# Performance work log

Hardware: AMD Instinct MI355X
Metric: run time of the kernel (lower is better)

## Reference

```python
import math
import jax, jax.numpy as jnp
import numpy as np

H = 8          # n_heads (params['h'])
TOPK_K = 2     # params['k']
TAU = 25       # moving-average window (params['tau'])


def ma_decomp(x, tau):
    """MADecompositionLayer: edge-pad by tau, centered moving average of width tau."""
    B, L, D = x.shape
    front = jnp.repeat(x[:, :1], tau, axis=1)
    back = jnp.repeat(x[:, -1:], tau, axis=1)
    padded = jnp.concatenate([front, x, back], axis=1)          # (B, L+2tau, D)
    cs = jnp.cumsum(padded, axis=1)
    cs = jnp.concatenate([jnp.zeros_like(cs[:, :1]), cs], axis=1)
    off = tau - (tau - 1) // 2  # start offset of the SAME-padded pool window
    trend = (cs[:, off + tau: off + tau + L] - cs[:, off: off + L]) / tau
    return x - trend, trend     # (seasonality, trend)


def corr_attention(x, Wq, bq, Wk, bk, Wv, bv, Wo, bo):
    """CorrLayer (inference path: per-sample top-k delay aggregation)."""
    B, L, D = x.shape
    dk = D // H
    # projections -> (B, h, d, L)
    q = (x @ Wq + bq).reshape(B, L, H, dk).transpose(0, 2, 3, 1)
    k = (x @ Wk + bk).reshape(B, L, H, dk).transpose(0, 2, 3, 1)
    v = (x @ Wv + bv).reshape(B, L, H, dk).transpose(0, 2, 3, 1)
    # FFT cross-correlation as written in the source:
    # corr = irfft(real = qr*kr, imag = -(qi*ki))
    qf = jnp.fft.rfft(q, axis=-1)
    kf = jnp.fft.rfft(k, axis=-1)
    spec = (qf.real * kf.real) - 1j * (qf.imag * kf.imag)
    corr = jnp.fft.irfft(spec, n=L, axis=-1)                    # (B, h, d, L)
    # top-k delay selection per sample
    top_k = min(int(TOPK_K * math.log(L)), L)
    mean_value = corr.mean(axis=(1, 2))                          # (B, L)
    weights, delay = jax.lax.top_k(mean_value, top_k)            # (B, topk)
    w = jax.nn.softmax(weights, axis=-1)                         # (B, topk)
    # circular-shift gather: values[..., (delay + arange(L)) % L]
    idx = (delay[:, :, None] + jnp.arange(L)[None, None, :]) % L  # (B, topk, L)
    rolled = jnp.take_along_axis(v[:, None], idx[:, :, None, None, :], axis=-1)  # (B, topk, h, d, L)
    agg = jnp.einsum('bt,bthdl->bhdl', w, rolled)                # (B, h, d, L)
    out = agg.transpose(0, 3, 1, 2).reshape(B, L, H * dk)        # (B, L, D)
    return out @ Wo + bo


def setup_inputs() -> dict:
    key = jax.random.key(0)
    ks = jax.random.split(key, 8)
    B, L, D, DFF = 8, 2048, 512, 2048
    s = 0.02
    return {
        'x':  jax.random.normal(ks[0], (B, L, D), jnp.float32),
        'Wq': jax.random.normal(ks[1], (D, D), jnp.float32) * s,
        'bq': jnp.zeros((D,), jnp.float32),
        'Wk': jax.random.normal(ks[2], (D, D), jnp.float32) * s,
        'bk': jnp.zeros((D,), jnp.float32),
        'Wv': jax.random.normal(ks[3], (D, D), jnp.float32) * s,
        'bv': jnp.zeros((D,), jnp.float32),
        'Wo': jax.random.normal(ks[4], (D, D), jnp.float32) * s,
        'bo': jnp.zeros((D,), jnp.float32),
        'W1': jax.random.normal(ks[5], (D, DFF), jnp.float32) * s,
        'W2': jax.random.normal(ks[6], (DFF, D), jnp.float32) * s,
    }


def reference(x, Wq, bq, Wk, bk, Wv, bv, Wo, bo, W1, W2):
    # Autoformer encoder layer: attn + residual, decomp, FFN, decomp
    attn_out = corr_attention(x, Wq, bq, Wk, bk, Wv, bv, Wo, bo)
    xr = x + attn_out                       # dropout_rate = 0.0
    s1, _ = ma_decomp(xr, TAU)
    y = jax.nn.relu(s1 @ W1) @ W2           # FFN (bias-free, as in Autoformer conv1d)
    s2, _ = ma_decomp(s1 + y, TAU)
    return s2
```

## Files before the change

### kernel.cpp

```cpp
#include <hip/hip_runtime.h>
#include <math.h>

namespace {
constexpr int kB = 8;
constexpr int kL = 2048;
constexpr int kD = 512;
constexpr int kTopk = 15;
constexpr int kLMask = 2047;
}

typedef unsigned short u16;
using f32x4 = __attribute__((ext_vector_type(4))) float;
using bf16x8 = __attribute__((ext_vector_type(8))) __bf16;

__device__ __forceinline__ u16 f2b(float f) {
  unsigned u = __float_as_uint(f);
  unsigned r = (u + 0x7fffu + ((u >> 16) & 1u)) >> 16;
  return (u16)r;
}
__device__ __forceinline__ float b2f(u16 u) {
  return __uint_as_float(((unsigned)u) << 16);
}

typedef __attribute__((address_space(3))) unsigned int lds_u32;
typedef __attribute__((address_space(1))) const unsigned int glb_u32;
__device__ __forceinline__ void gl2lds16(const void* g, void* l) {
  __builtin_amdgcn_global_load_lds((glb_u32*)g, (lds_u32*)l, 16, 0, 0);
}

template <int SPLIT, int RELU, int OUTF, int OUTB, int RES>
__global__ __launch_bounds__(256)
void mfma_gemm(const u16* __restrict__ A, const u16* __restrict__ Bt,
               const float* __restrict__ bias, const float* __restrict__ ResF,
               const u16* __restrict__ ResB, float* __restrict__ outF,
               u16* __restrict__ outB, int N, int K, int lda, int ldb, int nbn) {
  __shared__ u16 As[128 * 64];
  __shared__ u16 Bs[128 * 64];
  int lin = blockIdx.x;
  int split = 0;
  if (SPLIT) { split = lin >> 9; lin &= 511; }
  const int xcd = lin & 7;
  const int s = lin >> 3;
  const int q = s / nbn;
  const int bm = xcd * 16 + q;
  const int bn = s - q * nbn;
  const int tid = threadIdx.x;
  const int wave = tid >> 6;
  const int lane = tid & 63;
  const int ln = lane & 15;
  const int quad = lane >> 4;
  const int wm = (wave >> 1) * 64;
  const int wn = (wave & 1) * 64;
  const int srow = tid >> 3;
  const int scol = (tid & 7) * 8;

  const size_t koff = (size_t)split * K;
  const u16* Ab = A + koff + (size_t)(bm * 128) * lda + scol;
  const u16* Bb = Bt + koff + (size_t)(bn * 128) * ldb + scol;
  char* ldsA = (char*)As + wave * 1024;
  char* ldsB = (char*)Bs + wave * 1024;

  f32x4 acc[4][4];
#pragma unroll
  for (int i = 0; i < 4; ++i)
#pragma unroll
    for (int j = 0; j < 4; ++j) acc[i][j] = (f32x4){0.f, 0.f, 0.f, 0.f};

  for (int k0 = 0; k0 < K; k0 += 64) {
#pragma unroll
    for (int c = 0; c < 4; ++c) {
      gl2lds16(Ab + (size_t)(srow + 32 * c) * lda + k0, ldsA + c * 4096);
      gl2lds16(Bb + (size_t)(srow + 32 * c) * ldb + k0, ldsB + c * 4096);
    }
    __syncthreads();
#pragma unroll
    for (int kk = 0; kk < 2; ++kk) {
      bf16x8 af[4], bfr[4];
#pragma unroll
      for (int i = 0; i < 4; ++i)
        af[i] = *(const bf16x8*)(As + (wm + i * 16 + ln) * 64 + kk * 32 + quad * 8);
#pragma unroll
      for (int j = 0; j < 4; ++j)
        bfr[j] = *(const bf16x8*)(Bs + (wn + j * 16 + ln) * 64 + kk * 32 + quad * 8);
#pragma unroll
      for (int i = 0; i < 4; ++i)
#pragma unroll
        for (int j = 0; j < 4; ++j)
          acc[i][j] = __builtin_amdgcn_mfma_f32_16x16x32_bf16(bfr[j], af[i], acc[i][j], 0, 0, 0);
    }
    __syncthreads();
  }

  const size_t cbase = (size_t)split * ((size_t)16384 * N);
  const bool res2 = (RES == 2) && (!SPLIT || split == 0);
#pragma unroll
  for (int i = 0; i < 4; ++i) {
    const int row = bm * 128 + wm + i * 16 + ln;
#pragma unroll
    for (int j = 0; j < 4; ++j) {
      const int col = bn * 128 + wn + j * 16 + quad * 4;
      f32x4 v = acc[i][j];
      if (bias) {
        float4 bv = *(const float4*)(bias + col);
        v[0] += bv.x; v[1] += bv.y; v[2] += bv.z; v[3] += bv.w;
      }
      if (RES == 1) {
        float4 rv = *(const float4*)(ResF + (size_t)row * N + col);
        v[0] += rv.x; v[1] += rv.y; v[2] += rv.z; v[3] += rv.w;
      }
      if (RES == 2) {
        if (res2) {
          ushort4 rv = *(const ushort4*)(ResB + (size_t)row * N + col);
          v[0] += b2f(rv.x); v[1] += b2f(rv.y); v[2] += b2f(rv.z); v[3] += b2f(rv.w);
        }
      }
      if (RELU) {
#pragma unroll
        for (int r = 0; r < 4; ++r) v[r] = fmaxf(v[r], 0.f);
      }
      if (OUTF) {
        float4 o = {v[0], v[1], v[2], v[3]};
        *(float4*)(outF + cbase + (size_t)row * N + col) = o;
      }
      if (OUTB) {
        ushort4 o = {f2b(v[0]), f2b(v[1]), f2b(v[2]), f2b(v[3])};
        *(ushort4*)(outB + cbase + (size_t)row * N + col) = o;
      }
    }
  }
}

#define RDA(BUF, I, KK) \
  (*(const bf16x8*)&sm[BUF][0][arow + (I) * 1024 + ((KK) ? cx1 : cx0)])
#define RDB(BUF, J, KK) \
  (*(const bf16x8*)&sm[BUF][1][brow + (J) * 1024 + ((KK) ? cx1 : cx0)])
#define STAGE_A(BUF, Q, T) \
  gl2lds16(Ab + (size_t)(Q) * 64 * lda + (size_t)(T) * 64, \
           &sm[BUF][0][((Q) * 64 + wave * 8) * 64])
#define STAGE_B(BUF, Q, T) \
  gl2lds16(Bb + (size_t)(Q) * 64 * ldb + (size_t)(T) * 64, \
           &sm[BUF][1][((Q) * 64 + wave * 8) * 64])
#define MFMA1(i, j, kk, areg) \
  acc[i][j] = __builtin_amdgcn_mfma_f32_16x16x32_bf16(bf[j][kk], areg, acc[i][j], 0, 0, 0)
#define PHASE_MFMA(I0, A0k0, A0k1, A1k0, A1k1)                                 \
  MFMA1(I0, 0, 0, A0k0); MFMA1(I0, 1, 0, A0k0);                                \
  MFMA1(I0, 2, 0, A0k0); MFMA1(I0, 3, 0, A0k0);                                \
  MFMA1((I0) + 1, 0, 0, A1k0); MFMA1((I0) + 1, 1, 0, A1k0);                    \
  MFMA1((I0) + 1, 2, 0, A1k0); MFMA1((I0) + 1, 3, 0, A1k0);                    \
  MFMA1(I0, 0, 1, A0k1); MFMA1(I0, 1, 1, A0k1);                                \
  MFMA1(I0, 2, 1, A0k1); MFMA1(I0, 3, 1, A0k1);                                \
  MFMA1((I0) + 1, 0, 1, A1k1); MFMA1((I0) + 1, 1, 1, A1k1);                    \
  MFMA1((I0) + 1, 2, 1, A1k1); MFMA1((I0) + 1, 3, 1, A1k1)

#define GTILE(CUR, T)                                                          \
  {                                                                            \
    constexpr int NXT = (CUR) ^ 1;                                             \
    const bool hn = (T) + 1 < NT;                                              \
    const int tn = (T) + 1;                                                    \
    bf16x8 bf[4][2];                                                           \
    {                                                             \
      bf16x8 a00 = RDA(CUR, 0, 0), a01 = RDA(CUR, 0, 1);                       \
      bf16x8 a10 = RDA(CUR, 1, 0), a11 = RDA(CUR, 1, 1);                       \
      bf[0][0] = RDB(CUR, 0, 0); bf[0][1] = RDB(CUR, 0, 1);                    \
      bf[1][0] = RDB(CUR, 1, 0); bf[1][1] = RDB(CUR, 1, 1);                    \
      bf[2][0] = RDB(CUR, 2, 0); bf[2][1] = RDB(CUR, 2, 1);                    \
      bf[3][0] = RDB(CUR, 3, 0); bf[3][1] = RDB(CUR, 3, 1);                    \
      if (hn) { STAGE_B(NXT, 0, tn); STAGE_B(NXT, 1, tn); }                    \
      asm volatile("s_barrier" ::: "memory");                                  \
      __builtin_amdgcn_s_setprio(1);                                           \
      PHASE_MFMA(0, a00, a01, a10, a11);                                       \
      __builtin_amdgcn_s_setprio(0);                                           \
      asm volatile("s_barrier" ::: "memory");                                  \
    }                                                                          \
    {                                                             \
      bf16x8 a00 = RDA(CUR, 2, 0), a01 = RDA(CUR, 2, 1);                       \
      bf16x8 a10 = RDA(CUR, 3, 0), a11 = RDA(CUR, 3, 1);                       \
      if (hn) { STAGE_B(NXT, 2, tn); STAGE_B(NXT, 3, tn); }                    \
      asm volatile("s_barrier" ::: "memory");                                  \
      __builtin_amdgcn_s_setprio(1);                                           \
      PHASE_MFMA(2, a00, a01, a10, a11);                                       \
      __builtin_amdgcn_s_setprio(0);                                           \
      if (hn) { asm volatile("s_waitcnt vmcnt(4)" ::: "memory"); }             \
      else    { asm volatile("s_waitcnt vmcnt(0)" ::: "memory"); }             \
      asm volatile("s_barrier" ::: "memory");                                  \
    }                                                                          \
    {                                                             \
      bf16x8 a00 = RDA(CUR, 4, 0), a01 = RDA(CUR, 4, 1);                       \
      bf16x8 a10 = RDA(CUR, 5, 0), a11 = RDA(CUR, 5, 1);                       \
      if (hn) { STAGE_A(NXT, 0, tn); STAGE_A(NXT, 2, tn); }                    \
      asm volatile("s_barrier" ::: "memory");                                  \
      __builtin_amdgcn_s_setprio(1);                                           \
      PHASE_MFMA(4, a00, a01, a10, a11);                                       \
      __builtin_amdgcn_s_setprio(0);                                           \
      asm volatile("s_barrier" ::: "memory");                                  \
    }                                                                          \
    {                                                             \
      bf16x8 a00 = RDA(CUR, 6, 0), a01 = RDA(CUR, 6, 1);                       \
      bf16x8 a10 = RDA(CUR, 7, 0), a11 = RDA(CUR, 7, 1);                       \
      if (hn) { STAGE_A(NXT, 1, tn); STAGE_A(NXT, 3, tn); }                    \
      asm volatile("s_barrier" ::: "memory");                                  \
      __builtin_amdgcn_s_setprio(1);                                           \
      PHASE_MFMA(6, a00, a01, a10, a11);                                       \
      __builtin_amdgcn_s_setprio(0);                                           \
      if (hn) { asm volatile("s_waitcnt vmcnt(2)" ::: "memory"); }             \
      asm volatile("s_barrier" ::: "memory");                                  \
    }                                                                          \
  }

template <int SPLITK, int RELU, int HAS_BIAS, int OUTF, int RES>
__global__ __launch_bounds__(512, 2)
void gemm256(const u16* __restrict__ A, const u16* __restrict__ Bt,
             const float* __restrict__ bias, const u16* __restrict__ ResB,
             u16* __restrict__ outB, float* __restrict__ outF,
             int N, int K, int lda, int ldb, int nbn) {
  __shared__ u16 sm[2][2][256 * 64];
  const int lin = blockIdx.x;
  int bm, bn, split = 0;
  if (SPLITK) {
    const int xcd = lin & 7;
    const int s = lin >> 3;
    bm = xcd * 8 + (s & 7);
    bn = (s >> 3) & 1;
    split = s >> 4;
  } else {
    const int chunk = (int)gridDim.x >> 3;
    const int gid = (lin & 7) * chunk + (lin >> 3);
    bm = gid / nbn;
    bn = gid - bm * nbn;
  }

  const int tid = threadIdx.x;
  const int wave = tid >> 6;
  const int lane = tid & 63;
  const int ln = lane & 15;
  const int quad = lane >> 4;
  const int wm = (wave >> 2) * 128;
  const int wn = (wave & 3) * 64;

  const int srow = tid >> 3;
  const int schunk = (tid & 7) ^ (srow & 7);

  const size_t koff = (size_t)split * K;
  const u16* Ab = A + koff + (size_t)(bm * 256 + srow) * lda + schunk * 8;
  const u16* Bb = Bt + koff + (size_t)(bn * 256 + srow) * ldb + schunk * 8;

  const int cx0 = ((quad) ^ (ln & 7)) * 8;
  const int cx1 = ((4 | quad) ^ (ln & 7)) * 8;
  const int arow = (wm + ln) * 64;
  const int brow = (wn + ln) * 64;

  const int NT = K >> 6;

  f32x4 acc[8][4];
#pragma unroll
  for (int i = 0; i < 8; ++i)
#pragma unroll
    for (int j = 0; j < 4; ++j) acc[i][j] = (f32x4){0.f, 0.f, 0.f, 0.f};

  STAGE_B(0, 0, 0); STAGE_B(0, 1, 0); STAGE_B(0, 2, 0); STAGE_B(0, 3, 0);
  STAGE_A(0, 0, 0); STAGE_A(0, 2, 0); STAGE_A(0, 1, 0); STAGE_A(0, 3, 0);
  asm volatile("s_waitcnt vmcnt(2)" ::: "memory");
  asm volatile("s_barrier" ::: "memory");

  for (int t = 0; t < NT; t += 2) {
    GTILE(0, t);
    GTILE(1, t + 1);
  }

  const int col0 = bn * 256 + wn + quad * 4;
  const size_t cbase = (size_t)split * ((size_t)16384 * N);
#pragma unroll
  for (int i = 0; i < 8; ++i) {
    const size_t row = (size_t)(bm * 256 + wm + i * 16 + ln);
#pragma unroll
    for (int j = 0; j < 4; ++j) {
      const int col = col0 + j * 16;
      f32x4 v = acc[i][j];
      if (HAS_BIAS) {
        float4 bv = *(const float4*)(bias + col);
        v[0] += bv.x; v[1] += bv.y; v[2] += bv.z; v[3] += bv.w;
      }
      if (RES == 2) {
        if (split == 0) {
          ushort4 rv = *(const ushort4*)(ResB + row * N + col);
          v[0] += b2f(rv.x); v[1] += b2f(rv.y); v[2] += b2f(rv.z); v[3] += b2f(rv.w);
        }
      }
      if (RELU) {
        v[0] = fmaxf(v[0], 0.f); v[1] = fmaxf(v[1], 0.f);
        v[2] = fmaxf(v[2], 0.f); v[3] = fmaxf(v[3], 0.f);
      }
      if (OUTF) {
        float4 o = {v[0], v[1], v[2], v[3]};
        *(float4*)(outF + cbase + row * N + col) = o;
      } else {
        ushort4 o = {f2b(v[0]), f2b(v[1]), f2b(v[2]), f2b(v[3])};
        *(ushort4*)(outB + row * N + col) = o;
      }
    }
  }
}

#undef RDA
#undef RDB
#undef STAGE_A
#undef STAGE_B
#undef MFMA1
#undef PHASE_MFMA
#undef GTILE

__global__ __launch_bounds__(256)
void fft_corr(const u16* __restrict__ qkv, float* __restrict__ pA,
              float* __restrict__ pB) {
  __shared__ u16 stq[4 * 2048];
  __shared__ u16 stk[4 * 2048];
  __shared__ float re[2048];
  __shared__ float im[2048];
  const int blk = blockIdx.x;
  const int b = blk & 7;
  const int g = blk >> 3;
  const int t = threadIdx.x;
  const float PI = 3.14159265358979323846f;

  const u16* qb = qkv + (size_t)b * kL * 1536 + g * 4;
#pragma unroll
  for (int p = 0; p < 8; ++p) {
    const int row = p * 256 + t;
    *(ushort4*)&stq[row * 4] = *(const ushort4*)(qb + (size_t)row * 1536);
    *(ushort4*)&stk[row * 4] = *(const ushort4*)(qb + (size_t)row * 1536 + 512);
  }

  const int r = t & 31;
  float cA[4], sA[4], cB[2], sB[2], cC, sC;
  float cD[4], sD[4], cE[2], sE[2], cF, sF;
#pragma unroll
  for (int j = 0; j < 4; ++j)
    __sincosf(PI * (float)(t + 256 * j) * (1.f / 1024.f), &sA[j], &cA[j]);
#pragma unroll
  for (int j = 0; j < 2; ++j)
    __sincosf(PI * (float)(t + 256 * j) * (1.f / 512.f), &sB[j], &cB[j]);
  __sincosf(PI * (float)t * (1.f / 256.f), &sC, &cC);
#pragma unroll
  for (int j = 0; j < 4; ++j)
    __sincosf(PI * (float)(r + 32 * j) * (1.f / 128.f), &sD[j], &cD[j]);
#pragma unroll
  for (int j = 0; j < 2; ++j)
    __sincosf(PI * (float)(r + 32 * j) * (1.f / 64.f), &sE[j], &cE[j]);
  __sincosf(PI * (float)r * (1.f / 32.f), &sF, &cF);
  float sgn[5], cS[5], sS[5];
#pragma unroll
  for (int k = 0; k < 5; ++k) {
    const int m = 16 >> k;
    const bool hi = (t & m) != 0;
    float sv, cv;
    __sincosf(PI * (float)(t & (m - 1)) / (float)m, &sv, &cv);
    sgn[k] = hi ? -1.f : 1.f;
    cS[k] = hi ? cv : 1.f;
    sS[k] = hi ? sv : 0.f;
  }

  float accA[8], accB[8];
#pragma unroll
  for (int i = 0; i < 8; ++i) { accA[i] = 0.f; accB[i] = 0.f; }

  const int base2 = (t >> 5) * 256 + r;

#define BFLY(X, Y, CV, SV)                                              \
  { const float dr_ = er[X] - er[Y], di_ = ei[X] - ei[Y];               \
    er[X] += er[Y]; ei[X] += ei[Y];                                     \
    er[Y] = dr_ * (CV) + di_ * (SV); ei[Y] = di_ * (CV) - dr_ * (SV); }

#pragma unroll
  for (int c = 0; c < 4; ++c) {
    __syncthreads();
    float er[8], ei[8];
#pragma unroll
    for (int j = 0; j < 8; ++j) {
      er[j] = b2f(stq[(t + 256 * j) * 4 + c]);
      ei[j] = b2f(stk[(t + 256 * j) * 4 + c]);
    }
    BFLY(0, 4, cA[0], sA[0]); BFLY(1, 5, cA[1], sA[1]);
    BFLY(2, 6, cA[2], sA[2]); BFLY(3, 7, cA[3], sA[3]);
    BFLY(0, 2, cB[0], sB[0]); BFLY(1, 3, cB[1], sB[1]);
    BFLY(4, 6, cB[0], sB[0]); BFLY(5, 7, cB[1], sB[1]);
    BFLY(0, 1, cC, sC); BFLY(2, 3, cC, sC);
    BFLY(4, 5, cC, sC); BFLY(6, 7, cC, sC);
#pragma unroll
    for (int j = 0; j < 8; ++j) {
      re[t + 256 * j] = er[j];
      im[t + 256 * j] = ei[j];
    }
    __syncthreads();
#pragma unroll
    for (int j = 0; j < 8; ++j) {
      er[j] = re[base2 + 32 * j];
      ei[j] = im[base2 + 32 * j];
    }
    BFLY(0, 4, cD[0], sD[0]); BFLY(1, 5, cD[1], sD[1]);
    BFLY(2, 6, cD[2], sD[2]); BFLY(3, 7, cD[3], sD[3]);
    BFLY(0, 2, cE[0], sE[0]); BFLY(1, 3, cE[1], sE[1]);
    BFLY(4, 6, cE[0], sE[0]); BFLY(5, 7, cE[1], sE[1]);
    BFLY(0, 1, cF, sF); BFLY(2, 3, cF, sF);
    BFLY(4, 5, cF, sF); BFLY(6, 7, cF, sF);
#pragma unroll
    for (int k = 0; k < 5; ++k) {
      const int m = 16 >> k;
#pragma unroll
      for (int j = 0; j < 8; ++j) {
        const float otr = __shfl_xor(er[j], m, 64);
        const float oti = __shfl_xor(ei[j], m, 64);
        const float sr = otr + sgn[k] * er[j];
        const float si = oti + sgn[k] * ei[j];
        er[j] = sr * cS[k] + si * sS[k];
        ei[j] = si * cS[k] - sr * sS[k];
      }
    }
    __syncthreads();
#pragma unroll
    for (int j = 0; j < 8; ++j) {
      re[base2 + 32 * j] = er[j];
      im[base2 + 32 * j] = ei[j];
    }
    __syncthreads();
#pragma unroll
    for (int i = 0; i < 8; ++i) {
      const int pos = i * 256 + t;
      const int f = __brev((unsigned)pos) >> 21;
      if (f <= 1024) {
        const int fm = (2048 - f) & 2047;
        const int pm = __brev((unsigned)fm) >> 21;
        const float zr = re[pos], zi = im[pos];
        const float mr = re[pm], mi = im[pm];
        const float ReQ = 0.5f * (zr + mr);
        const float ImQ = 0.5f * (zi - mi);
        const float ReK = 0.5f * (zi + mi);
        const float ImK = 0.5f * (mr - zr);
        accA[i] += ReQ * ReK;
        accB[i] += ImQ * ImK;
      }
    }
  }
#undef BFLY

  float* pAb = pA + (size_t)blk * 1025;
  float* pBb = pB + (size_t)blk * 1025;
#pragma unroll
  for (int i = 0; i < 8; ++i) {
    const int pos = i * 256 + t;
    const int f = __brev((unsigned)pos) >> 21;
    if (f <= 1024) { pAb[f] = accA[i]; pBb[f] = accB[i]; }
  }
}

__global__ __launch_bounds__(256)
void reduceAB(const float* __restrict__ pA, const float* __restrict__ pB,
              float* __restrict__ Asp, float* __restrict__ Bsp) {
  const int b = blockIdx.x;
  const int f = blockIdx.y * 256 + threadIdx.x;
  if (f > 1024) return;
  float sa = 0.f, sb = 0.f;
  for (int g = 0; g < 128; ++g) {
    const size_t idx = (size_t)((g << 3) | b) * 1025 + f;
    sa += pA[idx];
    sb += pB[idx];
  }
  Asp[b * 1025 + f] = sa;
  Bsp[b * 1025 + f] = sb;
}

__global__ __launch_bounds__(256)
void ifft_meanv(const float* __restrict__ Asp, const float* __restrict__ Bsp,
                float* __restrict__ meanv) {
  __shared__ float re[2048];
  __shared__ float im[2048];
  __shared__ float twc[2047];
  __shared__ float tws[2047];
  const int b = blockIdx.x;
  const int t = threadIdx.x;
  for (int e = t; e < 2047; e += 256) {
    const int s = 31 - __clz(e + 1);
    const int m = 1 << s;
    const int j = e + 1 - m;
    float sv, cv;
    __sincosf((float)j * 3.14159265358979323846f / (float)m, &sv, &cv);
    twc[e] = cv;
    tws[e] = sv;
  }
#pragma unroll
  for (int i = 0; i < 8; ++i) {
    const int f = i * 256 + t;
    float Xr, Xi;
    if (f <= 1024) {
      Xr = Asp[b * 1025 + f];
      Xi = (f == 0 || f == 1024) ? 0.f : -Bsp[b * 1025 + f];
    } else {
      const int gg = 2048 - f;
      Xr = Asp[b * 1025 + gg];
      Xi = Bsp[b * 1025 + gg];
    }
    const int pos = __brev((unsigned)f) >> 21;
    re[pos] = Xr;
    im[pos] = Xi;
  }
  for (int s = 0; s <= 10; ++s) {
    __syncthreads();
    const int m = 1 << s;
    for (int p = 0; p < 4; ++p) {
      const int id = p * 256 + t;
      const int j = id & (m - 1);
      const int i0 = ((id >> s) << (s + 1)) + j;
      const int i1 = i0 + m;
      const int kk = (m - 1) + j;
      const float cv = twc[kk], sv = tws[kk];
      const float br = re[i1], bi = im[i1];
      const float tr = br * cv - bi * sv;
      const float ti = bi * cv + br * sv;
      const float ar = re[i0], ai = im[i0];
      re[i0] = ar + tr;
      im[i0] = ai + ti;
      re[i1] = ar - tr;
      im[i1] = ai - ti;
    }
  }
  __syncthreads();
#pragma unroll
  for (int i = 0; i < 8; ++i) {
    const int n = i * 256 + t;
    meanv[b * kL + n] = re[n] * (1.0f / (2048.0f * 512.0f));
  }
}

__global__ __launch_bounds__(256)
void cast_f2b_kernel(const float* __restrict__ X, u16* __restrict__ Y) {
  const int i = (blockIdx.x * 256 + threadIdx.x) * 4;
  float4 v = *(const float4*)(X + i);
  ushort4 o;
  o.x = f2b(v.x); o.y = f2b(v.y); o.z = f2b(v.z); o.w = f2b(v.w);
  *(ushort4*)(Y + i) = o;
}

__global__ __launch_bounds__(256)
void transpose4_kernel(const float* __restrict__ W0, const float* __restrict__ W1,
                       const float* __restrict__ W2, const float* __restrict__ W3,
                       u16* __restrict__ dst) {
  __shared__ float t[32][33];
  const int z = blockIdx.z;
  const float* W = z == 0 ? W0 : z == 1 ? W1 : z == 2 ? W2 : W3;
  u16* Wt = dst + (size_t)z * 512 * 512;
  const int k0 = blockIdx.y * 32, n0 = blockIdx.x * 32;
  const int tx = threadIdx.x & 31, ty = threadIdx.x >> 5;
  for (int r = ty; r < 32; r += 8)
    t[r][tx] = W[(size_t)(k0 + r) * 512 + n0 + tx];
  __syncthreads();
  for (int r = ty; r < 32; r += 8)
    Wt[(size_t)(n0 + r) * 512 + k0 + tx] = f2b(t[tx][r]);
}

__global__ __launch_bounds__(256)
void transpose_cast_kernel(const float* __restrict__ W, u16* __restrict__ Wt,
                           int K, int N) {
  __shared__ float t[32][33];
  const int k0 = blockIdx.y * 32, n0 = blockIdx.x * 32;
  const int tx = threadIdx.x & 31, ty = threadIdx.x >> 5;
  for (int r = ty; r < 32; r += 8)
    t[r][tx] = W[(size_t)(k0 + r) * N + n0 + tx];
  __syncthreads();
  for (int r = ty; r < 32; r += 8)
    Wt[(size_t)(n0 + r) * K + k0 + tx] = f2b(t[tx][r]);
}

__global__ void concat_bias_kernel(const float* __restrict__ bq,
                                   const float* __restrict__ bk,
                                   const float* __restrict__ bv,
                                   float* __restrict__ o) {
  const int i = blockIdx.x * 256 + threadIdx.x;
  const float* s = i < 512 ? bq : (i < 1024 ? bk : bv);
  o[i] = s[i & 511];
}

__global__ __launch_bounds__(256)
void topk1_kernel(const float* __restrict__ meanv, float* __restrict__ candv,
                  int* __restrict__ candi) {
  __shared__ float f[256];
  __shared__ float rv[256];
  __shared__ int ri[256];
  const int chunk = blockIdx.x;
  const int b = blockIdx.y;
  const int t = threadIdx.x;
  const int gi = chunk * 256 + t;
  f[t] = meanv[b * kL + gi];
  __syncthreads();
  const int obase = (b * 8 + chunk) * kTopk;
  for (int round = 0; round < kTopk; ++round) {
    rv[t] = f[t];
    ri[t] = gi;
    __syncthreads();
    for (int s = 128; s > 0; s >>= 1) {
      if (t < s) {
        const float v2 = rv[t + s];
        const int i2 = ri[t + s];
        if (v2 > rv[t] || (v2 == rv[t] && i2 < ri[t])) { rv[t] = v2; ri[t] = i2; }
      }
      __syncthreads();
    }
    if (t == 0) {
      candv[obase + round] = rv[0];
      candi[obase + round] = ri[0];
      f[ri[0] & 255] = -INFINITY;
    }
    __syncthreads();
  }
}

__global__ __launch_bounds__(128)
void topk2_kernel(const float* __restrict__ candv, const int* __restrict__ candi,
                  float* __restrict__ wts, int* __restrict__ dly) {
  __shared__ float f[128];
  __shared__ int fi[128];
  __shared__ float rv[128];
  __shared__ int ri[128];
  __shared__ float topv[kTopk];
  __shared__ int topi[kTopk];
  const int b = blockIdx.x;
  const int t = threadIdx.x;
  if (t < 120) {
    f[t] = candv[b * 120 + t];
    fi[t] = candi[b * 120 + t];
  } else {
    f[t] = -INFINITY;
    fi[t] = 1 << 30;
  }
  __syncthreads();
  for (int round = 0; round < kTopk; ++round) {
    rv[t] = f[t];
    ri[t] = t;
    __syncthreads();
    for (int s = 64; s > 0; s >>= 1) {
      if (t < s) {
        const float v2 = rv[t + s];
        const int i2 = ri[t + s];
        if (v2 > rv[t] || (v2 == rv[t] && fi[i2] < fi[ri[t]])) { rv[t] = v2; ri[t] = i2; }
      }
      __syncthreads();
    }
    if (t == 0) {
      topv[round] = rv[0];
      topi[round] = fi[ri[0]];
      f[ri[0]] = -INFINITY;
    }
    __syncthreads();
  }
  if (t == 0) {
    const float m = topv[0];
    float sum = 0.f;
    float e[kTopk];
    for (int i = 0; i < kTopk; ++i) { e[i] = expf(topv[i] - m); sum += e[i]; }
    for (int i = 0; i < kTopk; ++i) {
      wts[b * 16 + i] = e[i] / sum;
      dly[b * 16 + i] = topi[i];
    }
  }
}

__global__ __launch_bounds__(256)
void agg_kernel(const u16* __restrict__ qkv, const float* __restrict__ wts,
                const int* __restrict__ dly, u16* __restrict__ out) {
  __shared__ float w[16];
  __shared__ int dl[16];
  const int lin = blockIdx.x;
  const int b = lin & 7;
  if (threadIdx.x < kTopk) {
    w[threadIdx.x] = wts[b * 16 + threadIdx.x];
    dl[threadIdx.x] = dly[b * 16 + threadIdx.x];
  }
  __syncthreads();
  const int l = (lin >> 3) * 4 + (threadIdx.x >> 6);
  const int co = (threadIdx.x & 63) * 8;
  const u16* vb = qkv + (size_t)b * kL * 1536 + 1024 + co;
  float a[8] = {0.f, 0.f, 0.f, 0.f, 0.f, 0.f, 0.f, 0.f};
  for (int t = 0; t < kTopk; ++t) {
    const int row = (l + dl[t]) & kLMask;
    float4 rv = *(const float4*)(vb + (size_t)row * 1536);
    const u16* p = (const u16*)&rv;
    const float wt = w[t];
#pragma unroll
    for (int e = 0; e < 8; ++e) a[e] += wt * b2f(p[e]);
  }
  u16 ob[8];
#pragma unroll
  for (int e = 0; e < 8; ++e) ob[e] = f2b(a[e]);
  *(float4*)(out + ((size_t)b * kL + l) * kD + co) = *(const float4*)ob;
}

__global__ __launch_bounds__(256)
void decomp_b2b(const u16* __restrict__ X, u16* __restrict__ OB) {
  const int c = blockIdx.x * 256 + threadIdx.x;
  const int b = blockIdx.y;
  const int l0 = blockIdx.z * 64;
  const u16* base = X + (size_t)b * kL * kD + c;
  float sum = 0.f;
#pragma unroll
  for (int m = -12; m <= 12; ++m) {
    int lm = l0 + m;
    lm = lm < 0 ? 0 : (lm > kL - 1 ? kL - 1 : lm);
    sum += b2f(base[(size_t)lm * kD]);
  }
#pragma unroll 4
  for (int l = l0; l < l0 + 64; ++l) {
    const float val = b2f(base[(size_t)l * kD]);
    OB[((size_t)b * kL + l) * kD + c] = f2b(val - sum * (1.0f / 25.0f));
    const int la = l + 13 > kL - 1 ? kL - 1 : l + 13;
    const int lr = l - 12 < 0 ? 0 : l - 12;
    sum += b2f(base[(size_t)la * kD]) - b2f(base[(size_t)lr * kD]);
  }
}

__global__ __launch_bounds__(256)
void decomp_ff2(const float* __restrict__ X1, const float* __restrict__ X2,
                float* __restrict__ OF) {
  const int c = blockIdx.x * 256 + threadIdx.x;
  const int b = blockIdx.y;
  const int l0 = blockIdx.z * 64;
  const size_t off = (size_t)b * kL * kD + c;
  const float* b1 = X1 + off;
  const float* b2 = X2 + off;
  float sum = 0.f;
#pragma unroll
  for (int m = -12; m <= 12; ++m) {
    int lm = l0 + m;
    lm = lm < 0 ? 0 : (lm > kL - 1 ? kL - 1 : lm);
    sum += b1[(size_t)lm * kD] + b2[(size_t)lm * kD];
  }
#pragma unroll 4
  for (int l = l0; l < l0 + 64; ++l) {
    const float val = b1[(size_t)l * kD] + b2[(size_t)l * kD];
    OF[((size_t)b * kL + l) * kD + c] = val - sum * (1.0f / 25.0f);
    const int la = l + 13 > kL - 1 ? kL - 1 : l + 13;
    const int lr = l - 12 < 0 ? 0 : l - 12;
    sum += b1[(size_t)la * kD] + b2[(size_t)la * kD]
         - b1[(size_t)lr * kD] - b2[(size_t)lr * kD];
  }
}

extern "C" void kernel_launch(void* const* d_in, const int* in_sizes, int n_in,
                              void* d_out, int out_size, void* d_ws, size_t ws_size,
                              hipStream_t stream) {
  const float* x  = (const float*)d_in[0];
  const float* Wq = (const float*)d_in[1];
  const float* bq = (const float*)d_in[2];
  const float* Wk = (const float*)d_in[3];
  const float* bk = (const float*)d_in[4];
  const float* Wv = (const float*)d_in[5];
  const float* bv = (const float*)d_in[6];
  const float* Wo = (const float*)d_in[7];
  const float* bo = (const float*)d_in[8];
  const float* W1 = (const float*)d_in[9];
  const float* W2 = (const float*)d_in[10];
  float* out = (float*)d_out;

  const size_t MiB = 1u << 20;
  const size_t NBLD = (size_t)kB * kL * kD;
  char* base = (char*)d_ws;
  u16*   qkvb  = (u16*)(base);
  u16*   xb    = (u16*)(base + 48 * MiB);
  u16*   aggb  = xb;
  u16*   xrb   = (u16*)(base + 64 * MiB);
  u16*   s1b   = (u16*)(base + 80 * MiB);
  u16*   midb  = (u16*)(base + 96 * MiB);
  float* s2p   = (float*)(base);
  u16*   Wqkvt = (u16*)(base + 160 * MiB);
  u16*   Wot   = Wqkvt + 3 * 512 * 512;
  u16*   W1t   = (u16*)(base + 162 * MiB);
  u16*   W2t   = (u16*)(base + 164 * MiB);
  float* bqkv  = (float*)(base + 166 * MiB);
  float* Asp   = bqkv + 2048;
  float* Bsp   = Asp + kB * 1025;
  float* meanv = Bsp + kB * 1025;
  float* wtsf  = meanv + kB * kL;
  int*   dlyi  = (int*)(wtsf + kB * 16);
  float* candv = (float*)(dlyi + kB * 16);
  int*   candi = (int*)(candv + kB * 8 * kTopk);
  float* pA    = (float*)(base + 167 * MiB);
  float* pB    = (float*)(base + 172 * MiB);

  const dim3 blk(256);
  const dim3 blk512(512);

  cast_f2b_kernel<<<(int)(NBLD / 1024), blk, 0, stream>>>(x, xb);
  transpose4_kernel<<<dim3(16, 16, 4), blk, 0, stream>>>(Wq, Wk, Wv, Wo, Wqkvt);
  transpose_cast_kernel<<<dim3(64, 16), blk, 0, stream>>>(W1, W1t, 512, 2048);
  transpose_cast_kernel<<<dim3(16, 64), blk, 0, stream>>>(W2, W2t, 2048, 512);
  concat_bias_kernel<<<dim3(6), blk, 0, stream>>>(bq, bk, bv, bqkv);

  gemm256<0, 0, 1, 0, 0><<<dim3(384), blk512, 0, stream>>>(
      xb, Wqkvt, bqkv, nullptr, qkvb, nullptr, 1536, 512, 512, 512, 6);

  fft_corr<<<dim3(1024), blk, 0, stream>>>(qkvb, pA, pB);
  reduceAB<<<dim3(8, 5), blk, 0, stream>>>(pA, pB, Asp, Bsp);
  ifft_meanv<<<dim3(8), blk, 0, stream>>>(Asp, Bsp, meanv);

  topk1_kernel<<<dim3(8, 8), blk, 0, stream>>>(meanv, candv, candi);
  topk2_kernel<<<dim3(8), dim3(128), 0, stream>>>(candv, candi, wtsf, dlyi);

  agg_kernel<<<dim3(4096), blk, 0, stream>>>(qkvb, wtsf, dlyi, aggb);
  mfma_gemm<0, 0, 0, 1, 1><<<dim3(512), blk, 0, stream>>>(
      aggb, Wot, bo, x, nullptr, nullptr, xrb, 512, 512, 512, 512, 4);

  decomp_b2b<<<dim3(2, 8, 32), blk, 0, stream>>>(xrb, s1b);

  gemm256<0, 1, 0, 0, 0><<<dim3(512), blk512, 0, stream>>>(
      s1b, W1t, nullptr, nullptr, midb, nullptr, 2048, 512, 512, 512, 8);

  gemm256<1, 0, 0, 1, 2><<<dim3(256), blk512, 0, stream>>>(
      midb, W2t, nullptr, s1b, nullptr, s2p, 512, 1024, 2048, 2048, 2);

  decomp_ff2<<<dim3(2, 8, 32), blk, 0, stream>>>(s2p, s2p + NBLD, out);
}
```

Measured before the change: 435.4 us.

## Stage GEMM epilogue through swizzled LDS for coalesced stores; merge MFMA phases

The GEMM epilogue now writes accumulator tiles into shared memory with an XOR swizzle, in two chunks, then reads them back so each thread issues full 16-byte coalesced global stores of whole rows, instead of scattered 4-element stores. The main loop also merges pairs of MFMA phases: the next A fragments are read from LDS between MFMA groups, and two of the four barriers per tile are removed. This trades extra LDS traffic and barriers in the epilogue, plus longer register live ranges in the loop, for better global write efficiency and fewer sync points.

```diff
diff --git a/kernel.cpp b/kernel.cpp
--- a/kernel.cpp
+++ b/kernel.cpp
@@ -157,10 +157,10 @@
     constexpr int NXT = (CUR) ^ 1;                                             \
     const bool hn = (T) + 1 < NT;                                              \
     const int tn = (T) + 1;                                                    \
-    bf16x8 bf[4][2];                                                           \
-    {                                                             \
-      bf16x8 a00 = RDA(CUR, 0, 0), a01 = RDA(CUR, 0, 1);                       \
-      bf16x8 a10 = RDA(CUR, 1, 0), a11 = RDA(CUR, 1, 1);                       \
+    bf16x8 bf[4][2]; bf16x8 af[4][2];                                          \
+    {                                              \
+      af[0][0] = RDA(CUR, 0, 0); af[0][1] = RDA(CUR, 0, 1);                    \
+      af[1][0] = RDA(CUR, 1, 0); af[1][1] = RDA(CUR, 1, 1);                    \
       bf[0][0] = RDB(CUR, 0, 0); bf[0][1] = RDB(CUR, 0, 1);                    \
       bf[1][0] = RDB(CUR, 1, 0); bf[1][1] = RDB(CUR, 1, 1);                    \
       bf[2][0] = RDB(CUR, 2, 0); bf[2][1] = RDB(CUR, 2, 1);                    \
@@ -168,39 +168,27 @@
       if (hn) { STAGE_B(NXT, 0, tn); STAGE_B(NXT, 1, tn); }                    \
       asm volatile("s_barrier" ::: "memory");                                  \
       __builtin_amdgcn_s_setprio(1);                                           \
-      PHASE_MFMA(0, a00, a01, a10, a11);                                       \
-      __builtin_amdgcn_s_setprio(0);                                           \
-      asm volatile("s_barrier" ::: "memory");                                  \
-    }                                                                          \
-    {                                                             \
-      bf16x8 a00 = RDA(CUR, 2, 0), a01 = RDA(CUR, 2, 1);                       \
-      bf16x8 a10 = RDA(CUR, 3, 0), a11 = RDA(CUR, 3, 1);                       \
+      PHASE_MFMA(0, af[0][0], af[0][1], af[1][0], af[1][1]);                   \
+      af[2][0] = RDA(CUR, 2, 0); af[2][1] = RDA(CUR, 2, 1);                    \
+      af[3][0] = RDA(CUR, 3, 0); af[3][1] = RDA(CUR, 3, 1);                    \
       if (hn) { STAGE_B(NXT, 2, tn); STAGE_B(NXT, 3, tn); }                    \
-      asm volatile("s_barrier" ::: "memory");                                  \
-      __builtin_amdgcn_s_setprio(1);                                           \
-      PHASE_MFMA(2, a00, a01, a10, a11);                                       \
+      PHASE_MFMA(2, af[2][0], af[2][1], af[3][0], af[3][1]);                   \
       __builtin_amdgcn_s_setprio(0);                                           \
       if (hn) { asm volatile("s_waitcnt vmcnt(4)" ::: "memory"); }             \
       else    { asm volatile("s_waitcnt vmcnt(0)" ::: "memory"); }             \
       asm volatile("s_barrier" ::: "memory");                                  \
     }                                                                          \
-    {                                                             \
-      bf16x8 a00 = RDA(CUR, 4, 0), a01 = RDA(CUR, 4, 1);                       \
-      bf16x8 a10 = RDA(CUR, 5, 0), a11 = RDA(CUR, 5, 1);                       \
+    {                                              \
+      af[0][0] = RDA(CUR, 4, 0); af[0][1] = RDA(CUR, 4, 1);                    \
+      af[1][0] = RDA(CUR, 5, 0); af[1][1] = RDA(CUR, 5, 1);                    \
       if (hn) { STAGE_A(NXT, 0, tn); STAGE_A(NXT, 2, tn); }                    \
       asm volatile("s_barrier" ::: "memory");                                  \
       __builtin_amdgcn_s_setprio(1);                                           \
-      PHASE_MFMA(4, a00, a01, a10, a11);                                       \
-      __builtin_amdgcn_s_setprio(0);                                           \
-      asm volatile("s_barrier" ::: "memory");                                  \
-    }                                                                          \
-    {                                                             \
-      bf16x8 a00 = RDA(CUR, 6, 0), a01 = RDA(CUR, 6, 1);                       \
-      bf16x8 a10 = RDA(CUR, 7, 0), a11 = RDA(CUR, 7, 1);                       \
+      PHASE_MFMA(4, af[0][0], af[0][1], af[1][0], af[1][1]);                   \
+      af[2][0] = RDA(CUR, 6, 0); af[2][1] = RDA(CUR, 6, 1);                    \
+      af[3][0] = RDA(CUR, 7, 0); af[3][1] = RDA(CUR, 7, 1);                    \
       if (hn) { STAGE_A(NXT, 1, tn); STAGE_A(NXT, 3, tn); }                    \
-      asm volatile("s_barrier" ::: "memory");                                  \
-      __builtin_amdgcn_s_setprio(1);                                           \
-      PHASE_MFMA(6, a00, a01, a10, a11);                                       \
+      PHASE_MFMA(6, af[2][0], af[2][1], af[3][0], af[3][1]);                   \
       __builtin_amdgcn_s_setprio(0);                                           \
       if (hn) { asm volatile("s_waitcnt vmcnt(2)" ::: "memory"); }             \
       asm volatile("s_barrier" ::: "memory");                                  \
@@ -269,33 +257,75 @@
 
   const int col0 = bn * 256 + wn + quad * 4;
   const size_t cbase = (size_t)split * ((size_t)16384 * N);
-#pragma unroll
-  for (int i = 0; i < 8; ++i) {
-    const size_t row = (size_t)(bm * 256 + wm + i * 16 + ln);
-#pragma unroll
-    for (int j = 0; j < 4; ++j) {
-      const int col = col0 + j * 16;
-      f32x4 v = acc[i][j];
-      if (HAS_BIAS) {
-        float4 bv = *(const float4*)(bias + col);
-        v[0] += bv.x; v[1] += bv.y; v[2] += bv.z; v[3] += bv.w;
-      }
-      if (RES == 2) {
-        if (split == 0) {
-          ushort4 rv = *(const ushort4*)(ResB + row * N + col);
-          v[0] += b2f(rv.x); v[1] += b2f(rv.y); v[2] += b2f(rv.z); v[3] += b2f(rv.w);
+  const int wmh = wm >> 1;
+
+#pragma unroll
+  for (int chunk = 0; chunk < 2; ++chunk) {
+    if (chunk) {
+      asm volatile("s_waitcnt lgkmcnt(0)" ::: "memory");
+      asm volatile("s_barrier" ::: "memory");
+    }
+#pragma unroll
+    for (int i2 = 0; i2 < 4; ++i2) {
+      const int i = chunk * 4 + i2;
+      const int lr = wmh + i2 * 16 + ln;
+      const size_t row = (size_t)(bm * 256 + wm + i * 16 + ln);
+#pragma unroll
+      for (int j = 0; j < 4; ++j) {
+        const int col = col0 + j * 16;
+        const int ct = wn + j * 16 + quad * 4;
+        f32x4 v = acc[i][j];
+        if (HAS_BIAS) {
+          float4 bv = *(const float4*)(bias + col);
+          v[0] += bv.x; v[1] += bv.y; v[2] += bv.z; v[3] += bv.w;
         }
-      }
-      if (RELU) {
-        v[0] = fmaxf(v[0], 0.f); v[1] = fmaxf(v[1], 0.f);
-        v[2] = fmaxf(v[2], 0.f); v[3] = fmaxf(v[3], 0.f);
-      }
-      if (OUTF) {
-        float4 o = {v[0], v[1], v[2], v[3]};
-        *(float4*)(outF + cbase + row * N + col) = o;
-      } else {
-        ushort4 o = {f2b(v[0]), f2b(v[1]), f2b(v[2]), f2b(v[3])};
-        *(ushort4*)(outB + row * N + col) = o;
+        if (RES == 2) {
+          if (split == 0) {
+            ushort4 rv = *(const ushort4*)(ResB + row * N + col);
+            v[0] += b2f(rv.x); v[1] += b2f(rv.y); v[2] += b2f(rv.z); v[3] += b2f(rv.w);
+          }
+        }
+        if (RELU) {
+          v[0] = fmaxf(v[0], 0.f); v[1] = fmaxf(v[1], 0.f);
+          v[2] = fmaxf(v[2], 0.f); v[3] = fmaxf(v[3], 0.f);
+        }
+        if (OUTF) {
+          float* scrF = (float*)&sm[0][0][0];
+          const int off = (lr * 1024 + ct * 4) ^ ((lr & 7) << 4);
+          *(f32x4*)((char*)scrF + off) = v;
+        } else {
+          u16* scr = (u16*)&sm[0][0][0];
+          ushort4 o = {f2b(v[0]), f2b(v[1]), f2b(v[2]), f2b(v[3])};
+          const int off = (lr * 512 + ct * 2) ^ ((lr & 7) << 4);
+          *(ushort4*)((char*)scr + off) = o;
+        }
+      }
+    }
+    asm volatile("s_waitcnt lgkmcnt(0)" ::: "memory");
+    asm volatile("s_barrier" ::: "memory");
+    if (OUTF) {
+      const float* scrF = (const float*)&sm[0][0][0];
+#pragma unroll
+      for (int it = 0; it < 16; ++it) {
+        const int idx = it * 512 + tid;
+        const int r = idx >> 6;
+        const int u = idx & 63;
+        const int src = r * 1024 + ((u ^ (r & 7)) << 4);
+        f32x4 d = *(const f32x4*)((const char*)scrF + src);
+        const size_t grow = (size_t)(bm * 256 + ((r >> 6) << 7) + chunk * 64 + (r & 63));
+        *((f32x4*)(outF + cbase + grow * N + bn * 256) + u) = d;
+      }
+    } else {
+      const u16* scr = (const u16*)&sm[0][0][0];
+#pragma unroll
+      for (int it = 0; it < 8; ++it) {
+        const int idx = it * 512 + tid;
+        const int r = idx >> 5;
+        const int u = idx & 31;
+        const int src = r * 512 + ((u ^ (r & 7)) << 4);
+        f32x4 d = *(const f32x4*)((const char*)scr + src);
+        const size_t grow = (size_t)(bm * 256 + ((r >> 6) << 7) + chunk * 64 + (r & 63));
+        *(f32x4*)((char*)(outB + grow * N + bn * 256) + u * 16) = d;
       }
     }
   }
```

Measured after the change: 420.5 us. -3.4%, faster.
